# Kernel optimization log

Measured on AMD Instinct MI355X. Metric: run time of the kernel, lower is better.

The kernel has to match this reference:

```python
import jax, jax.numpy as jnp
import numpy as np

N, F, H, E = 20000, 512, 8, 320000
D = F // H
SCALING = D ** (-0.5)


def _layernorm(x, g, b, eps=1e-5):
    mu = jnp.mean(x, axis=-1, keepdims=True)
    var = jnp.var(x, axis=-1, keepdims=True)
    return (x - mu) * jax.lax.rsqrt(var + eps) * g + b


def setup_inputs() -> dict:
    key = jax.random.key(0)
    ks = jax.random.split(key, 12)
    feat = jax.random.normal(ks[0], (N, F), dtype=jnp.float32)
    edge_src = jax.random.randint(ks[1], (E,), 0, N, dtype=jnp.int32)
    edge_dst = jax.random.randint(ks[2], (E,), 0, N, dtype=jnp.int32)
    # self-loops on the first N edges so every node has in-degree >= 1
    loops = jnp.arange(N, dtype=jnp.int32)
    edge_src = edge_src.at[:N].set(loops)
    edge_dst = edge_dst.at[:N].set(loops)
    s = 1.0 / np.sqrt(F)
    def w(k, shape, scale=s):
        return jax.random.normal(k, shape, dtype=jnp.float32) * scale
    return {
        "feat": feat, "edge_src": edge_src, "edge_dst": edge_dst,
        "Wq": w(ks[3], (F, F)), "Wk": w(ks[4], (F, F)), "Wv": w(ks[5], (F, F)),
        "Wnode": w(ks[6], (F, F)), "Wskip": w(ks[7], (F, F)),
        "Wgate": w(ks[8], (3 * F, 1), scale=1.0 / np.sqrt(3 * F)),
        "ln1_g": jnp.ones((F,), jnp.float32), "ln1_b": jnp.zeros((F,), jnp.float32),
        "ln2_g": jnp.ones((F,), jnp.float32), "ln2_b": jnp.zeros((F,), jnp.float32),
        "W1": w(ks[9], (F, F)), "W2": w(ks[10], (F, F)),
    }


def reference(feat, edge_src, edge_dst, Wq, Wk, Wv, Wnode, Wskip, Wgate,
              ln1_g, ln1_b, ln2_g, ln2_b, W1, W2):
    # --- attention (GraphMultiAttentionV2, use_efeats=False, eval mode) ---
    q = (feat @ Wq).reshape(N, H, D)
    k = (feat @ Wk).reshape(N, H, D)
    v = (feat @ Wv).reshape(N, H, D)
    # u_dot_v: per-edge per-head dot product  [E, H]
    logits = jnp.einsum('ehd,ehd->eh', q[edge_src], k[edge_dst])
    logits = jnp.clip(logits, -5.0, 5.0) / SCALING  # faithful: a / scaling
    # edge softmax grouped by destination node
    m = jax.ops.segment_max(logits, edge_dst, num_segments=N)  # [N, H]
    ex = jnp.exp(logits - m[edge_dst])
    denom = jax.ops.segment_sum(ex, edge_dst, num_segments=N)
    sa = ex / denom[edge_dst]  # [E, H]
    # u_mul_e + sum aggregation
    msg = v[edge_src] * sa[..., None]  # [E, H, D]
    agg = jax.ops.segment_sum(msg, edge_dst, num_segments=N).reshape(N, F)
    rst = agg @ Wnode
    # --- gated residual ---
    skip = feat @ Wskip
    gate = jax.nn.sigmoid(jnp.concatenate([rst, skip, rst - skip], axis=-1) @ Wgate)
    h = _layernorm(rst * gate + skip * (1.0 - gate), ln1_g, ln1_b)
    # --- FFN + residual ---
    ffn = jax.nn.relu(_layernorm(h, ln2_g, ln2_b) @ W1) @ W2
    return h + ffn
```

## Files before the change

kernel.cpp:

```cpp
#include <hip/hip_runtime.h>
#include <hip/hip_bf16.h>
#include <hip/hip_fp16.h>

#define NN 20000
#define FD 512
#define NH 8
#define NE 320000
#define MP 20096

typedef unsigned int u32;
typedef unsigned short u16;
typedef __bf16 bf16x8 __attribute__((ext_vector_type(8)));
typedef _Float16 f16x8 __attribute__((ext_vector_type(8)));
typedef float f32x4 __attribute__((ext_vector_type(4)));

#define AS1 __attribute__((address_space(1)))
#define AS3 __attribute__((address_space(3)))

__device__ __forceinline__ u16 f2bf(float f) {
  __hip_bfloat16 h = __float2bfloat16(f);
  union { __hip_bfloat16 b; u16 u; } c; c.b = h; return c.u;
}
__device__ __forceinline__ float bf2f(u32 u) { return __uint_as_float(u << 16); }
__device__ __forceinline__ u16 f2h(float f) {
  union { __half h; u16 u; } c; c.h = __float2half(f); return c.u;
}
__device__ __forceinline__ void gl_lds16(const void* g, void* l) {
  __builtin_amdgcn_global_load_lds((AS1 void*)const_cast<void*>(g), (AS3 void*)l, 16, 0, 0);
}
__device__ __forceinline__ void up_h4(uint2 w, float* f) {
  union { u32 u; __half2 h; } c;
  c.u = w.x; float2 t0 = __half22float2(c.h); f[0]=t0.x; f[1]=t0.y;
  c.u = w.y; float2 t1 = __half22float2(c.h); f[2]=t1.x; f[3]=t1.y;
}

__global__ __launch_bounds__(256) void k_wprep(const float* __restrict__ feat,
    const float* __restrict__ Wq, const float* __restrict__ Wk,
    const float* __restrict__ Wv, const float* __restrict__ Wsk,
    const float* __restrict__ Wn, const float* __restrict__ W1,
    const float* __restrict__ W2, const float* __restrict__ Wg,
    u16* __restrict__ Af, u16* __restrict__ Bqkvs, u16* __restrict__ Bnt,
    u16* __restrict__ B1t, u16* __restrict__ B2t,
    float* __restrict__ gA, float* __restrict__ gB)
{
  int idx = blockIdx.x * 256 + threadIdx.x;
  if (idx < MP * FD / 4) {
    size_t i = (size_t)idx * 4;
    float4 v = make_float4(0.f, 0.f, 0.f, 0.f);
    if (i < (size_t)NN * FD) v = *(const float4*)(feat + i);
    *(ushort4*)(Af + i) = make_ushort4(f2h(v.x), f2h(v.y), f2h(v.z), f2h(v.w));
    return;
  }
  idx -= MP * FD / 4;
  if (idx < 2048 * 512) {
    int n = idx >> 9, k = idx & 511;
    float v;
    if (n < 512)       v = Wq[k * 512 + n];
    else if (n < 1024) v = Wk[k * 512 + (n - 512)];
    else if (n < 1536) v = Wv[k * 512 + (n - 1024)];
    else               v = Wsk[k * 512 + (n - 1536)];
    Bqkvs[idx] = f2h(v);
    return;
  }
  idx -= 2048 * 512;
  if (idx < 512 * 512) { int n = idx >> 9, k = idx & 511; Bnt[idx] = f2bf(Wn[k * 512 + n]); return; }
  idx -= 512 * 512;
  if (idx < 512 * 512) { int n = idx >> 9, k = idx & 511; B1t[idx] = f2bf(W1[k * 512 + n]); return; }
  idx -= 512 * 512;
  if (idx < 512 * 512) { int n = idx >> 9, k = idx & 511; B2t[idx] = f2bf(W2[k * 512 + n]); return; }
  idx -= 512 * 512;
  if (idx < 512) {
    gA[idx] = Wg[idx] + Wg[2 * 512 + idx];
    gB[idx] = Wg[512 + idx] - Wg[2 * 512 + idx];
  }
}

template<int NCOLS, int MODE, int FP16>
__global__ __launch_bounds__(256, 2) void k_gemm(
    const u16* __restrict__ A, const u16* __restrict__ B,
    float* __restrict__ Cf, u16* __restrict__ Cb, u16* __restrict__ Cb2,
    u16* __restrict__ Cb3, int Mreal)
{
  const long brow = (long)blockIdx.x * 128;
  if (brow >= MP) return;
  __shared__ u16 sA[128 * 64];
  __shared__ u16 sB[128 * 64];
  const int tid = threadIdx.x, lane = tid & 63, w = tid >> 6;
  const int wr = w >> 1, wc = w & 1;
  const long bcol = (long)blockIdx.y * 128;
  const int rl = lane >> 3, cl = (lane & 7) * 8;
  f32x4 acc[4][4] = {};
  for (int kt = 0; kt < FD; kt += 64) {
#pragma unroll
    for (int i = 0; i < 4; i++) {
      int r0 = i * 32 + w * 8;
      gl_lds16(A + (brow + r0 + rl) * FD + kt + cl, &sA[r0 * 64]);
      gl_lds16(B + (bcol + r0 + rl) * FD + kt + cl, &sB[r0 * 64]);
    }
    __syncthreads();
#pragma unroll
    for (int kk = 0; kk < 64; kk += 32) {
      const int ro = kk + (lane >> 4) * 8;
#pragma unroll
      for (int m = 0; m < 4; m++) {
        const u16* pa = &sA[(wr*64 + m*16 + (lane&15))*64 + ro];
#pragma unroll
        for (int n = 0; n < 4; n++) {
          const u16* pb = &sB[(wc*64 + n*16 + (lane&15))*64 + ro];
          if constexpr (FP16)
            acc[m][n] = __builtin_amdgcn_mfma_f32_16x16x32_f16(
                *(const f16x8*)pa, *(const f16x8*)pb, acc[m][n], 0, 0, 0);
          else
            acc[m][n] = __builtin_amdgcn_mfma_f32_16x16x32_bf16(
                *(const bf16x8*)pa, *(const bf16x8*)pb, acc[m][n], 0, 0, 0);
        }
      }
    }
    __syncthreads();
  }
#pragma unroll
  for (int m = 0; m < 4; m++) {
    long row0 = brow + wr * 64 + m * 16 + (lane >> 4) * 4;
#pragma unroll
    for (int n = 0; n < 4; n++) {
      long col = bcol + wc * 64 + n * 16 + (lane & 15);
#pragma unroll
      for (int j = 0; j < 4; j++) {
        long row = row0 + j;
        if (row < Mreal) {
          float v = acc[m][n][j];
          if constexpr (MODE == 1) Cb[row * NCOLS + col] = f2bf(fmaxf(v, 0.f));
          else if constexpr (MODE == 2) Cb[row * NCOLS + col] = f2bf(v);
          else if constexpr (MODE == 3) Cf[row * NCOLS + col] += v;
          else {
            if (col < 512)       Cb[row * 1024 + col] = f2h(v);
            else if (col < 1024) Cb2[row * 512 + (col - 512)] = f2h(v);
            else if (col < 1536) Cb[row * 1024 + 512 + (col - 1024)] = f2h(v);
            else                 Cb3[row * 512 + (col - 1536)] = f2bf(v);
          }
        }
      }
    }
  }
}

__global__ __launch_bounds__(256) void k_deg(const int* __restrict__ dst, int* __restrict__ deg)
{
  int e = blockIdx.x * 256 + threadIdx.x;
  if (e < NE) atomicAdd(&deg[dst[e]], 1);
}

__global__ void k_scan(const int* __restrict__ deg, int* __restrict__ offa)
{
  __shared__ int buf[1024];
  __shared__ int carry;
  if (threadIdx.x == 0) { carry = 0; offa[0] = 0; }
  __syncthreads();
  for (int base = 0; base < NN; base += 1024) {
    int i = base + threadIdx.x;
    int v = (i < NN) ? deg[i] : 0;
    buf[threadIdx.x] = v;
    __syncthreads();
    for (int s = 1; s < 1024; s <<= 1) {
      int t = (threadIdx.x >= s) ? buf[threadIdx.x - s] : 0;
      __syncthreads();
      buf[threadIdx.x] += t;
      __syncthreads();
    }
    if (i < NN) offa[i + 1] = carry + buf[threadIdx.x];
    __syncthreads();
    if (threadIdx.x == 0) carry += buf[1023];
    __syncthreads();
  }
}

__global__ __launch_bounds__(256) void k_scatter(const int* __restrict__ src, const int* __restrict__ dst,
    const int* __restrict__ offa, int* __restrict__ cnt, int* __restrict__ esrcs)
{
  int e = blockIdx.x * 256 + threadIdx.x;
  if (e >= NE) return;
  int d = dst[e];
  int p = offa[d] + atomicAdd(&cnt[d], 1);
  esrcs[p] = src[e];
}

__global__ __launch_bounds__(256) void k_edge(const int* __restrict__ offa,
    const int* __restrict__ esrcs, const u16* __restrict__ QV,
    const u16* __restrict__ Kb, u16* __restrict__ aggb)
{
  int wid = blockIdx.x * 4 + (threadIdx.x >> 6);
  int nd = wid >> 1, half = wid & 1;
  int lane = threadIdx.x & 63;
  if (nd >= MP) return;
  const int off = half * 256 + lane * 4;
  u16* op = aggb + (size_t)nd * FD + off;
  if (nd >= NN) { *(ushort4*)op = make_ushort4(0, 0, 0, 0); return; }
  uint2 kw = *(const uint2*)(Kb + (size_t)nd * 512 + off);
  float kx[4]; up_h4(kw, kx);
  int b0 = offa[nd], b1 = offa[nd + 1];
  float den = 0.f, a0 = 0.f, a1 = 0.f, a2 = 0.f, a3 = 0.f;
  for (int p = b0; p < b1; p += 8) {
    int ss[8]; uint2 qw[8], vw[8];
#pragma unroll
    for (int u = 0; u < 8; u++) { int ix = p + u; ss[u] = esrcs[ix < b1 ? ix : b1 - 1]; }
#pragma unroll
    for (int u = 0; u < 8; u++) {
      const u16* r = QV + (size_t)ss[u] * 1024 + off;
      qw[u] = *(const uint2*)r;
      vw[u] = *(const uint2*)(r + 512);
    }
#pragma unroll
    for (int u = 0; u < 8; u++) {
      float qx[4]; up_h4(qw[u], qx);
      float d = qx[0]*kx[0] + qx[1]*kx[1] + qx[2]*kx[2] + qx[3]*kx[3];
      d += __shfl_xor(d, 1); d += __shfl_xor(d, 2);
      d += __shfl_xor(d, 4); d += __shfl_xor(d, 8);
      float ex = __expf(fminf(fmaxf(d, -5.f), 5.f) * 8.f - 40.f);
      ex = (p + u < b1) ? ex : 0.f;
      den += ex;
      float vx[4]; up_h4(vw[u], vx);
      a0 += ex * vx[0]; a1 += ex * vx[1]; a2 += ex * vx[2]; a3 += ex * vx[3];
    }
  }
  float rd = 1.f / den;
  *(ushort4*)op = make_ushort4(f2bf(a0*rd), f2bf(a1*rd), f2bf(a2*rd), f2bf(a3*rd));
}

__device__ __forceinline__ float blkred(float v, float* sb)
{
#pragma unroll
  for (int s = 1; s < 64; s <<= 1) v += __shfl_xor(v, s);
  __syncthreads();
  if ((threadIdx.x & 63) == 0) sb[threadIdx.x >> 6] = v;
  __syncthreads();
  return sb[0] + sb[1];
}

__global__ __launch_bounds__(128) void k_gate_ln(const u16* __restrict__ rstb, const u16* __restrict__ skpb,
    const float* __restrict__ gA, const float* __restrict__ gB,
    const float* __restrict__ g1, const float* __restrict__ b1,
    const float* __restrict__ g2, const float* __restrict__ b2,
    float* __restrict__ hout, u16* __restrict__ h2b)
{
  __shared__ float sb[2];
  const int t = threadIdx.x;
  const size_t base = (size_t)blockIdx.x * FD + t * 4;
  ushort4 ru = *(const ushort4*)(rstb + base);
  ushort4 su = *(const ushort4*)(skpb + base);
  float r0 = bf2f(ru.x), r1 = bf2f(ru.y), r2 = bf2f(ru.z), r3 = bf2f(ru.w);
  float s0 = bf2f(su.x), s1 = bf2f(su.y), s2 = bf2f(su.z), s3 = bf2f(su.w);
  float4 av = *(const float4*)(gA + t * 4);
  float4 bv = *(const float4*)(gB + t * 4);
  float gd = r0*av.x + r1*av.y + r2*av.z + r3*av.w
           + s0*bv.x + s1*bv.y + s2*bv.z + s3*bv.w;
  float tot = blkred(gd, sb);
  float g = 1.f / (1.f + __expf(-tot));
  float x0 = g*r0 + (1.f-g)*s0;
  float x1 = g*r1 + (1.f-g)*s1;
  float x2 = g*r2 + (1.f-g)*s2;
  float x3 = g*r3 + (1.f-g)*s3;
  float m1 = blkred(x0+x1+x2+x3, sb) * (1.f/FD);
  float d0 = x0-m1, d1 = x1-m1, d2 = x2-m1, d3 = x3-m1;
  float v1 = blkred(d0*d0+d1*d1+d2*d2+d3*d3, sb) * (1.f/FD);
  float rs = rsqrtf(v1 + 1e-5f);
  float4 G1 = *(const float4*)(g1 + t*4);
  float4 Bb1 = *(const float4*)(b1 + t*4);
  float h0 = d0*rs*G1.x + Bb1.x;
  float h1 = d1*rs*G1.y + Bb1.y;
  float h2 = d2*rs*G1.z + Bb1.z;
  float h3 = d3*rs*G1.w + Bb1.w;
  *(float4*)(hout + base) = make_float4(h0, h1, h2, h3);
  float m2 = blkred(h0+h1+h2+h3, sb) * (1.f/FD);
  float e0 = h0-m2, e1 = h1-m2, e2 = h2-m2, e3 = h3-m2;
  float v2 = blkred(e0*e0+e1*e1+e2*e2+e3*e3, sb) * (1.f/FD);
  float rs2 = rsqrtf(v2 + 1e-5f);
  float4 G2 = *(const float4*)(g2 + t*4);
  float4 Bb2 = *(const float4*)(b2 + t*4);
  *(ushort4*)(h2b + base) = make_ushort4(
      f2bf(e0*rs2*G2.x + Bb2.x), f2bf(e1*rs2*G2.y + Bb2.y),
      f2bf(e2*rs2*G2.z + Bb2.z), f2bf(e3*rs2*G2.w + Bb2.w));
}

extern "C" void kernel_launch(void* const* d_in, const int* in_sizes, int n_in,
                              void* d_out, int out_size, void* d_ws, size_t ws_size,
                              hipStream_t stream)
{
  const float* feat = (const float*)d_in[0];
  const int* e_src = (const int*)d_in[1];
  const int* e_dst = (const int*)d_in[2];
  const float* Wq  = (const float*)d_in[3];
  const float* Wk  = (const float*)d_in[4];
  const float* Wv  = (const float*)d_in[5];
  const float* Wn  = (const float*)d_in[6];
  const float* Wsk = (const float*)d_in[7];
  const float* Wg  = (const float*)d_in[8];
  const float* l1g = (const float*)d_in[9];
  const float* l1b = (const float*)d_in[10];
  const float* l2g = (const float*)d_in[11];
  const float* l2b = (const float*)d_in[12];
  const float* W1  = (const float*)d_in[13];
  const float* W2  = (const float*)d_in[14];

  char* ws = (char*)d_ws;
  size_t o = 0;
  auto al = [&](size_t b) { char* r = ws + o; o = (o + b + 255) & ~(size_t)255; return r; };

  u16* Af    = (u16*)al((size_t)MP * FD * 2);
  u16* Bqkvs = (u16*)al((size_t)2048 * FD * 2);
  u16* Bnt   = (u16*)al((size_t)FD * FD * 2);
  u16* B1t   = (u16*)al((size_t)FD * FD * 2);
  u16* B2t   = (u16*)al((size_t)FD * FD * 2);
  float* gA  = (float*)al(FD * 4);
  float* gB  = (float*)al(FD * 4);
  u16* QV    = (u16*)al((size_t)MP * 1024 * 2);
  u16* Kb    = (u16*)al((size_t)MP * FD * 2);
  u16* SKIPb = (u16*)al((size_t)MP * FD * 2);
  u16* aggb  = (u16*)al((size_t)MP * FD * 2);
  u16* h2b   = (u16*)al((size_t)MP * FD * 2);
  int* deg   = (int*)al((size_t)2 * NN * 4);
  int* cnt   = deg + NN;
  int* offa  = (int*)al((size_t)(NN + 1) * 4);
  int* esrcs = (int*)al((size_t)NE * 4);
  if (o > ws_size) return;
  u16* rstb = Kb;
  u16* midb = Af;
  float* out = (float*)d_out;

  hipMemsetAsync(deg, 0, (size_t)2 * NN * 4, stream);

  {
    int total = MP * FD / 4 + 2048 * 512 + 3 * 512 * 512 + 512;
    k_wprep<<<dim3((total + 255) / 256), 256, 0, stream>>>(feat, Wq, Wk, Wv, Wsk, Wn, W1, W2, Wg,
        Af, Bqkvs, Bnt, B1t, B2t, gA, gB);
  }

  k_gemm<2048, 6, 1><<<dim3(160, 16), 256, 0, stream>>>(Af, Bqkvs, nullptr, QV, Kb, SKIPb, MP);

  k_deg<<<dim3((NE + 255) / 256), 256, 0, stream>>>(e_dst, deg);
  k_scan<<<dim3(1), 1024, 0, stream>>>(deg, offa);
  k_scatter<<<dim3((NE + 255) / 256), 256, 0, stream>>>(e_src, e_dst, offa, cnt, esrcs);
  k_edge<<<dim3(MP / 2), 256, 0, stream>>>(offa, esrcs, QV, Kb, aggb);

  k_gemm<512, 2, 0><<<dim3(160, 4), 256, 0, stream>>>(aggb, Bnt, nullptr, rstb, nullptr, nullptr, MP);
  k_gate_ln<<<dim3(NN), 128, 0, stream>>>(rstb, SKIPb, gA, gB, l1g, l1b, l2g, l2b, out, h2b);
  k_gemm<512, 1, 0><<<dim3(160, 4), 256, 0, stream>>>(h2b, B1t, nullptr, midb, nullptr, nullptr, MP);
  k_gemm<512, 3, 0><<<dim3(160, 4), 256, 0, stream>>>(midb, B2t, out, nullptr, nullptr, nullptr, NN);
}
```

Measured before the change: 339.5 us.

## Double-buffer GEMM K-tiles with smaller LDS tiles and use wave-shuffle scan

Result: faster. 330.7 us (-2.6%).

```diff
diff --git a/kernel.cpp b/kernel.cpp
--- a/kernel.cpp
+++ b/kernel.cpp
@@ -76,47 +76,51 @@
 }
 
 template<int NCOLS, int MODE, int FP16>
-__global__ __launch_bounds__(256, 2) void k_gemm(
+__global__ __launch_bounds__(256, 4) void k_gemm(
     const u16* __restrict__ A, const u16* __restrict__ B,
     float* __restrict__ Cf, u16* __restrict__ Cb, u16* __restrict__ Cb2,
     u16* __restrict__ Cb3, int Mreal)
 {
   const long brow = (long)blockIdx.x * 128;
   if (brow >= MP) return;
-  __shared__ u16 sA[128 * 64];
-  __shared__ u16 sB[128 * 64];
+  __shared__ u16 sA[2][128 * 32];
+  __shared__ u16 sB[2][128 * 32];
   const int tid = threadIdx.x, lane = tid & 63, w = tid >> 6;
   const int wr = w >> 1, wc = w & 1;
   const long bcol = (long)blockIdx.y * 128;
-  const int rl = lane >> 3, cl = (lane & 7) * 8;
+  const int srl = tid >> 2, scl = (tid & 3) * 8;
+
+  auto stage = [&](int b, int kt) {
+#pragma unroll
+    for (int s = 0; s < 2; s++) {
+      gl_lds16(A + (brow + s * 64 + srl) * FD + kt + scl, &sA[b][s * 2048 + w * 512]);
+      gl_lds16(B + (bcol + s * 64 + srl) * FD + kt + scl, &sB[b][s * 2048 + w * 512]);
+    }
+  };
+
   f32x4 acc[4][4] = {};
-  for (int kt = 0; kt < FD; kt += 64) {
-#pragma unroll
-    for (int i = 0; i < 4; i++) {
-      int r0 = i * 32 + w * 8;
-      gl_lds16(A + (brow + r0 + rl) * FD + kt + cl, &sA[r0 * 64]);
-      gl_lds16(B + (bcol + r0 + rl) * FD + kt + cl, &sB[r0 * 64]);
-    }
-    __syncthreads();
-#pragma unroll
-    for (int kk = 0; kk < 64; kk += 32) {
-      const int ro = kk + (lane >> 4) * 8;
-#pragma unroll
-      for (int m = 0; m < 4; m++) {
-        const u16* pa = &sA[(wr*64 + m*16 + (lane&15))*64 + ro];
-#pragma unroll
-        for (int n = 0; n < 4; n++) {
-          const u16* pb = &sB[(wc*64 + n*16 + (lane&15))*64 + ro];
-          if constexpr (FP16)
-            acc[m][n] = __builtin_amdgcn_mfma_f32_16x16x32_f16(
-                *(const f16x8*)pa, *(const f16x8*)pb, acc[m][n], 0, 0, 0);
-          else
-            acc[m][n] = __builtin_amdgcn_mfma_f32_16x16x32_bf16(
-                *(const bf16x8*)pa, *(const bf16x8*)pb, acc[m][n], 0, 0, 0);
-        }
+  stage(0, 0);
+  __syncthreads();
+  int cur = 0;
+  const int ro = (lane >> 4) * 8;
+  for (int kt = 0; kt < FD; kt += 32) {
+    if (kt + 32 < FD) stage(cur ^ 1, kt + 32);
+#pragma unroll
+    for (int m = 0; m < 4; m++) {
+      const u16* pa = &sA[cur][(wr * 64 + m * 16 + (lane & 15)) * 32 + ro];
+#pragma unroll
+      for (int n = 0; n < 4; n++) {
+        const u16* pb = &sB[cur][(wc * 64 + n * 16 + (lane & 15)) * 32 + ro];
+        if constexpr (FP16)
+          acc[m][n] = __builtin_amdgcn_mfma_f32_16x16x32_f16(
+              *(const f16x8*)pa, *(const f16x8*)pb, acc[m][n], 0, 0, 0);
+        else
+          acc[m][n] = __builtin_amdgcn_mfma_f32_16x16x32_bf16(
+              *(const bf16x8*)pa, *(const bf16x8*)pb, acc[m][n], 0, 0, 0);
       }
     }
     __syncthreads();
+    cur ^= 1;
   }
 #pragma unroll
   for (int m = 0; m < 4; m++) {
@@ -152,24 +156,35 @@
 
 __global__ void k_scan(const int* __restrict__ deg, int* __restrict__ offa)
 {
-  __shared__ int buf[1024];
+  __shared__ int wsum[16];
   __shared__ int carry;
-  if (threadIdx.x == 0) { carry = 0; offa[0] = 0; }
+  const int tid = threadIdx.x, lane = tid & 63, wid = tid >> 6;
+  if (tid == 0) { carry = 0; offa[0] = 0; }
   __syncthreads();
   for (int base = 0; base < NN; base += 1024) {
-    int i = base + threadIdx.x;
-    int v = (i < NN) ? deg[i] : 0;
-    buf[threadIdx.x] = v;
-    __syncthreads();
-    for (int s = 1; s < 1024; s <<= 1) {
-      int t = (threadIdx.x >= s) ? buf[threadIdx.x - s] : 0;
-      __syncthreads();
-      buf[threadIdx.x] += t;
-      __syncthreads();
-    }
-    if (i < NN) offa[i + 1] = carry + buf[threadIdx.x];
-    __syncthreads();
-    if (threadIdx.x == 0) carry += buf[1023];
+    int i = base + tid;
+    int s = (i < NN) ? deg[i] : 0;
+#pragma unroll
+    for (int d = 1; d < 64; d <<= 1) {
+      int t = __shfl_up(s, d);
+      if (lane >= d) s += t;
+    }
+    if (lane == 63) wsum[wid] = s;
+    __syncthreads();
+    if (tid < 16) {
+      int ws = wsum[tid];
+#pragma unroll
+      for (int d = 1; d < 16; d <<= 1) {
+        int t = __shfl_up(ws, d, 16);
+        if (tid >= d) ws += t;
+      }
+      wsum[tid] = ws;
+    }
+    __syncthreads();
+    int add = carry + (wid ? wsum[wid - 1] : 0);
+    if (i < NN) offa[i + 1] = add + s;
+    __syncthreads();
+    if (tid == 0) carry += wsum[15];
     __syncthreads();
   }
 }
```
